# Kernel tuning notes

Hardware: AMD Instinct MI355X
Metric: run time of the kernel (lower is better)

## Reference

```python
import jax, jax.numpy as jnp
import numpy as np

D_MODEL = 1024
N_HEAD = 16
HEAD_DIM = D_MODEL // N_HEAD


def setup_inputs() -> dict:
    key = jax.random.key(0)
    k1, k2, k3 = jax.random.split(key, 3)
    B, T = 2, 2048
    x = jax.random.normal(k1, (B, T, D_MODEL), dtype=jnp.float32)
    # nn.MultiheadAttention packed in-projection: (3*D, D), xavier-like scale
    w_in = jax.random.normal(k2, (3 * D_MODEL, D_MODEL), dtype=jnp.float32) * (1.0 / np.sqrt(D_MODEL))
    b_in = jnp.zeros((3 * D_MODEL,), dtype=jnp.float32)
    w_out = jax.random.normal(k3, (D_MODEL, D_MODEL), dtype=jnp.float32) * (1.0 / np.sqrt(D_MODEL))
    b_out = jnp.zeros((D_MODEL,), dtype=jnp.float32)
    return {"x": x, "w_in": w_in, "b_in": b_in, "w_out": w_out, "b_out": b_out}


def reference(x, w_in, b_in, w_out, b_out):
    B, T, D = x.shape
    H, hd = N_HEAD, HEAD_DIM
    # packed QKV projection (torch Linear convention: y = x @ W.T + b)
    qkv = x @ w_in.T + b_in                      # [B, T, 3D]
    q, k, v = jnp.split(qkv, 3, axis=-1)
    # [B, H, T, hd]
    q = q.reshape(B, T, H, hd).transpose(0, 2, 1, 3)
    k = k.reshape(B, T, H, hd).transpose(0, 2, 1, 3)
    v = v.reshape(B, T, H, hd).transpose(0, 2, 1, 3)
    scale = 1.0 / np.sqrt(hd).astype(np.float32)
    scores = jnp.einsum("bhqd,bhkd->bhqk", q * scale, k)  # [B, H, T, T]
    causal = jnp.tril(jnp.ones((T, T), dtype=bool))
    scores = jnp.where(causal, scores, jnp.finfo(scores.dtype).min)
    attn = jax.nn.softmax(scores, axis=-1)
    ctx = jnp.einsum("bhqk,bhkd->bhqd", attn, v)           # [B, H, T, hd]
    ctx = ctx.transpose(0, 2, 1, 3).reshape(B, T, D)
    return ctx @ w_out.T + b_out
```

## Files before the change

kernel.cpp:

```cpp
#include <hip/hip_runtime.h>


#define T_SEQ 2048
#define D_MODEL 1024
#define NEG_BIG (-1.0e30f)
#define Q_SCALE 0.18033688f

typedef float f32x4 __attribute__((ext_vector_type(4)));
typedef short s16x8 __attribute__((ext_vector_type(8)));
typedef __bf16 bf16x8 __attribute__((ext_vector_type(8)));

__device__ __forceinline__ f32x4 mfma16(s16x8 a, s16x8 b, f32x4 c) {
    return __builtin_amdgcn_mfma_f32_16x16x32_bf16(
        __builtin_bit_cast(bf16x8, a), __builtin_bit_cast(bf16x8, b), c, 0, 0, 0);
}

__device__ __forceinline__ short f2bf(float f) {
    unsigned int u = __float_as_uint(f);
    u += 0x7fffu + ((u >> 16) & 1u);
    return (short)(u >> 16);
}
__device__ __forceinline__ float bf2f(short s) {
    return __uint_as_float(((unsigned int)(unsigned short)s) << 16);
}
__device__ __forceinline__ unsigned cvt_pk_bf16(float lo, float hi) {
    unsigned r;
    asm("v_cvt_pk_bf16_f32 %0, %1, %2" : "=v"(r) : "v"(lo), "v"(hi));
    return r;
}

__device__ __forceinline__ void async_lds16(const short* g, short* l) {
    __builtin_amdgcn_global_load_lds(
        (const __attribute__((address_space(1))) unsigned int*)g,
        (__attribute__((address_space(3))) unsigned int*)l, 16, 0, 0);
}

#define N_X   4194304
#define N_WI  3145728
#define N_BI  3072
#define N_WO  1048576
#define N_BO  1024
#define V_X   (N_X  / 4)
#define V_WI  (N_WI / 4)
#define V_BI  (N_BI / 4)
#define V_WO  (N_WO / 4)
#define V_BO  (N_BO / 4)
#define V_TOT (V_X + V_WI + V_BI + V_WO + V_BO)

__global__ __launch_bounds__(256) void canon_all_kernel(
    const float* __restrict__ x, const float* __restrict__ wi,
    const float* __restrict__ bi, const float* __restrict__ wo,
    const float* __restrict__ bo,
    short* __restrict__ xb, short* __restrict__ wib, short* __restrict__ bib,
    short* __restrict__ wob, short* __restrict__ bob)
{
    int i = blockIdx.x * 256 + threadIdx.x;
    if (i >= V_TOT) return;
    const float* src; short* dst; int off;
    if      (i < V_X)                    { src = x;  dst = xb;  off = i; }
    else if (i < V_X+V_WI)               { src = wi; dst = wib; off = i - V_X; }
    else if (i < V_X+V_WI+V_BI)          { src = bi; dst = bib; off = i - V_X - V_WI; }
    else if (i < V_X+V_WI+V_BI+V_WO)     { src = wo; dst = wob; off = i - V_X - V_WI - V_BI; }
    else                                 { src = bo; dst = bob; off = i - V_X - V_WI - V_BI - V_WO; }
    float4 v = ((const float4*)src)[off];
    short4 o = { f2bf(v.x), f2bf(v.y), f2bf(v.z), f2bf(v.w) };
    ((short4*)dst)[off] = o;
}

__global__ __launch_bounds__(512, 6) void gemm_qkv_kernel(
    const short* __restrict__ A, const short* __restrict__ B,
    const short* __restrict__ bias,
    short* __restrict__ qo, short* __restrict__ ko, short* __restrict__ vto)
{
    const int K = 1024;
    alignas(16) __shared__ short As[128][32];
    alignas(16) __shared__ short Bs[128][32];
    const int m0 = blockIdx.x * 128;
    const int n0 = blockIdx.y * 128;
    const int tid = threadIdx.x;
    const int lane = tid & 63;
    const int w = tid >> 6;
    const int wm = (w & 3) * 32;
    const int wn = (w >> 2) * 64;
    const int quad = lane >> 4, l16 = lane & 15;

    f32x4 acc[2][4];
    const f32x4 zero = {0.f, 0.f, 0.f, 0.f};
#pragma unroll
    for (int i = 0; i < 2; ++i)
#pragma unroll
        for (int j = 0; j < 4; ++j) acc[i][j] = zero;

    const int lrow = lane >> 2;
    const int lcol = (lane & 3) * 8;
    const short* gA = &A[(m0 + w*16 + lrow) * K + lcol];
    const short* gB = &B[(n0 + w*16 + lrow) * K + lcol];
    short* lA = &As[w*16][0];
    short* lB = &Bs[w*16][0];

    for (int k0 = 0; k0 < K; k0 += 32) {
        __syncthreads();
        async_lds16(gA + k0, lA);
        async_lds16(gB + k0, lB);
        __syncthreads();

        s16x8 af[2], bfr[4];
#pragma unroll
        for (int i = 0; i < 2; ++i) af[i]  = *(const s16x8*)&As[wm + i*16 + l16][quad*8];
#pragma unroll
        for (int j = 0; j < 4; ++j) bfr[j] = *(const s16x8*)&Bs[wn + j*16 + l16][quad*8];
#pragma unroll
        for (int i = 0; i < 2; ++i)
#pragma unroll
            for (int j = 0; j < 4; ++j)
                acc[i][j] = mfma16(af[i], bfr[j], acc[i][j]);
    }

#pragma unroll
    for (int j = 0; j < 4; ++j) {
        int n = n0 + wn + j*16 + l16;
        float bi = bf2f(bias[n]);
        int which = n >> 10;
        int h = (n >> 6) & 15, d = n & 63;
        if (which < 2) {
            short* dst = (which == 0) ? qo : ko;
            float scl = (which == 0) ? Q_SCALE : 1.0f;
#pragma unroll
            for (int i = 0; i < 2; ++i) {
#pragma unroll
                for (int r = 0; r < 4; ++r) {
                    int m = m0 + wm + i*16 + quad*4 + r;
                    int b = m >> 11, t = m & 2047;
                    float v = (acc[i][j][r] + bi) * scl;
                    dst[(((b*16 + h) * 2048) + t) * 64 + d] = f2bf(v);
                }
            }
        } else {
#pragma unroll
            for (int i = 0; i < 2; ++i) {
                int m = m0 + wm + i*16 + quad*4;
                int b = m >> 11, t0 = m & 2047;
                short4 o4 = { f2bf(acc[i][j][0] + bi), f2bf(acc[i][j][1] + bi),
                              f2bf(acc[i][j][2] + bi), f2bf(acc[i][j][3] + bi) };
                *(short4*)&vto[(((size_t)(b*16 + h) * 64) + d) * 2048 + t0] = o4;
            }
        }
    }
}

__global__ __launch_bounds__(512) void attn_kernel(
    const short* __restrict__ Q, const short* __restrict__ K,
    const short* __restrict__ Vt, short* __restrict__ ctx)
{
    alignas(16) __shared__ short Ks2[2][64][64];
    alignas(16) __shared__ short Vs2[2][64][64];
    alignas(16) __shared__ short Pl[8][16][72];

    const int bh = blockIdx.x;
    const int j  = blockIdx.y;
    const int tid = threadIdx.x;
    const int w = tid >> 6, lane = tid & 63;
    const int quad = lane >> 4, l16 = lane & 15;
    const int b = bh >> 4, h = bh & 15;

    const int isB = w >> 2;
    const int wq  = w & 3;
    const int qt  = isB ? (31 - j) : j;
    const int qbase  = qt * 64;
    const int qbaseA = j * 64;
    const int qbaseB = (31 - j) * 64;

    const short* Qb  = Q  + bh * T_SEQ * 64;
    const short* Kb  = K  + bh * T_SEQ * 64;
    const short* Vbt = Vt + (size_t)bh * 64 * T_SEQ;

    const int qg = qbase + wq*16 + l16;
    const short* qrow = Qb + qg * 64;
    const s16x8 qa0 = *(const s16x8*)(qrow + quad*8);
    const s16x8 qa1 = *(const s16x8*)(qrow + 32 + quad*8);

    const s16x8 ones = { (short)0x3F80, (short)0x3F80, (short)0x3F80, (short)0x3F80,
                         (short)0x3F80, (short)0x3F80, (short)0x3F80, (short)0x3F80 };

    const f32x4 zero = {0.f, 0.f, 0.f, 0.f};
    f32x4 o[4];
#pragma unroll
    for (int dt = 0; dt < 4; ++dt) o[dt] = zero;
    f32x4 ls = zero;

    const int srow   = w*8 + (lane >> 3);
    const int schunk = ((lane & 7) ^ (lane >> 3)) * 8;
    short* kdst0 = &Ks2[0][w*8][0];
    short* kdst1 = &Ks2[1][w*8][0];
    short* vdst0 = &Vs2[0][w*8][0];
    short* vdst1 = &Vs2[1][w*8][0];

    const int csw = (l16 & 7) * 8;

    async_lds16(&Kb[srow * 64 + schunk], kdst0);
    async_lds16(&Vbt[(size_t)srow * T_SEQ + schunk], vdst0);

    int cur = 0;
    for (int s0 = 0; s0 <= qbaseB; s0 += 64) {
        __syncthreads();

        if (s0 + 64 <= qbaseB) {
            async_lds16(&Kb[(s0 + 64 + srow) * 64 + schunk], cur ? kdst0 : kdst1);
            async_lds16(&Vbt[(size_t)srow * T_SEQ + s0 + 64 + schunk], cur ? vdst0 : vdst1);
        }

        const bool act = isB || (s0 <= qbaseA);
        if (act) {
#pragma unroll
            for (int sub = 0; sub < 4; ++sub) {
                s16x8 ka0 = *(const s16x8*)&Ks2[cur][sub*16 + l16][(quad*8) ^ csw];
                s16x8 ka1 = *(const s16x8*)&Ks2[cur][sub*16 + l16][(32 + quad*8) ^ csw];
                __builtin_amdgcn_s_setprio(1);
                f32x4 S = mfma16(ka1, qa1, mfma16(ka0, qa0, zero));
                __builtin_amdgcn_s_setprio(0);
                if (s0 == qbase) {
                    int sb = s0 + sub*16 + quad*4;
#pragma unroll
                    for (int r = 0; r < 4; ++r)
                        if (sb + r > qg) S[r] = NEG_BIG;
                }
                float p0 = exp2f(S[0]), p1 = exp2f(S[1]);
                float p2 = exp2f(S[2]), p3 = exp2f(S[3]);
                uint2 pk;
                pk.x = cvt_pk_bf16(p0, p1);
                pk.y = cvt_pk_bf16(p2, p3);
                *(uint2*)&Pl[w][l16][sub*16 + quad*4] = pk;
            }

            s16x8 pb0 = *(const s16x8*)&Pl[w][l16][quad*8];
            s16x8 pb1 = *(const s16x8*)&Pl[w][l16][32 + quad*8];
            __builtin_amdgcn_s_setprio(1);
            ls = mfma16(ones, pb1, mfma16(ones, pb0, ls));
#pragma unroll
            for (int dt = 0; dt < 4; ++dt) {
                s16x8 va0 = *(const s16x8*)&Vs2[cur][dt*16 + l16][(quad*8) ^ csw];
                s16x8 va1 = *(const s16x8*)&Vs2[cur][dt*16 + l16][(32 + quad*8) ^ csw];
                o[dt] = mfma16(va1, pb1, mfma16(va0, pb0, o[dt]));
            }
            __builtin_amdgcn_s_setprio(0);
        }
        cur ^= 1;
    }

    float inv = 1.0f / ls[0];
    int base = (b * T_SEQ + qg) * D_MODEL + h * 64;
#pragma unroll
    for (int dt = 0; dt < 4; ++dt) {
        uint2 pk;
        pk.x = cvt_pk_bf16(o[dt][0] * inv, o[dt][1] * inv);
        pk.y = cvt_pk_bf16(o[dt][2] * inv, o[dt][3] * inv);
        *(uint2*)&ctx[base + dt*16 + quad*4] = pk;
    }
}

__global__ __launch_bounds__(512, 4) void gemm_out_kernel(
    const short* __restrict__ A, const short* __restrict__ B,
    const short* __restrict__ bias, float* __restrict__ out)
{
    const int K = 1024;
    alignas(16) __shared__ short As[128][32];
    alignas(16) __shared__ short Bs[64][32];
    const int m0 = blockIdx.x * 128;
    const int n0 = blockIdx.y * 64;
    const int tid = threadIdx.x;
    const int lane = tid & 63;
    const int w = tid >> 6;
    const int wm = (w & 3) * 32;
    const int wn = (w >> 2) * 32;
    const int quad = lane >> 4, l16 = lane & 15;

    f32x4 acc[2][2];
    const f32x4 zero = {0.f, 0.f, 0.f, 0.f};
#pragma unroll
    for (int i = 0; i < 2; ++i)
#pragma unroll
        for (int j = 0; j < 2; ++j) acc[i][j] = zero;

    const int lrow = lane >> 2;
    const int lcol = (lane & 3) * 8;
    const short* gA = &A[(m0 + w*16 + lrow) * K + lcol];
    const short* gB = &B[(n0 + (w & 3)*16 + lrow) * K + lcol];
    short* lA = &As[w*16][0];
    short* lB = &Bs[(w & 3)*16][0];
    const bool stageB = (w < 4);

    for (int k0 = 0; k0 < K; k0 += 32) {
        __syncthreads();
        async_lds16(gA + k0, lA);
        if (stageB) async_lds16(gB + k0, lB);
        __syncthreads();

        s16x8 af[2], bfr[2];
#pragma unroll
        for (int i = 0; i < 2; ++i) af[i]  = *(const s16x8*)&As[wm + i*16 + l16][quad*8];
#pragma unroll
        for (int j = 0; j < 2; ++j) bfr[j] = *(const s16x8*)&Bs[wn + j*16 + l16][quad*8];
#pragma unroll
        for (int i = 0; i < 2; ++i)
#pragma unroll
            for (int j = 0; j < 2; ++j)
                acc[i][j] = mfma16(af[i], bfr[j], acc[i][j]);
    }

#pragma unroll
    for (int j = 0; j < 2; ++j) {
        int n = n0 + wn + j*16 + l16;
        float bi = bf2f(bias[n]);
#pragma unroll
        for (int i = 0; i < 2; ++i) {
#pragma unroll
            for (int r = 0; r < 4; ++r) {
                int m = m0 + wm + i*16 + quad*4 + r;
                out[m * 1024 + n] = acc[i][j][r] + bi;
            }
        }
    }
}

extern "C" void kernel_launch(void* const* d_in, const int* in_sizes, int n_in,
                              void* d_out, int out_size, void* d_ws, size_t ws_size,
                              hipStream_t stream) {
    float* out = (float*)d_out;
    char* ws = (char*)d_ws;

    const size_t MB = 1u << 20;
    short* xb     = (short*)(ws);
    short* w_inb  = (short*)(ws + 8*MB);
    short* b_inb  = (short*)(ws + 14*MB);
    short* w_outb = (short*)(ws + 15*MB);
    short* b_outb = (short*)(ws + 17*MB);
    short* qb     = (short*)(ws + 18*MB);
    short* kb     = (short*)(ws + 26*MB);
    short* vtb    = (short*)(ws + 34*MB);
    short* ctxb   = (short*)(ws + 42*MB);

    canon_all_kernel<<<(V_TOT + 255) / 256, 256, 0, stream>>>(
        (const float*)d_in[0], (const float*)d_in[1], (const float*)d_in[2],
        (const float*)d_in[3], (const float*)d_in[4],
        xb, w_inb, b_inb, w_outb, b_outb);

    gemm_qkv_kernel<<<dim3(32, 24), 512, 0, stream>>>(xb, w_inb, b_inb, qb, kb, vtb);
    attn_kernel<<<dim3(32, 16), 512, 0, stream>>>(qb, kb, vtb, ctxb);
    gemm_out_kernel<<<dim3(32, 16), 512, 0, stream>>>(ctxb, w_outb, b_outb, out);
}
```

Measured before the change: 172.0 us.

## Replace async double-buffered LDS loads with register-staged single buffer

Drops the async global-to-LDS double buffer with XOR swizzling in the attention kernel. K/V tiles are now prefetched into registers, written into a single padded LDS tile (row stride 72), and guarded by an extra barrier each iteration. This halves K/V shared memory and removes the swizzle arithmetic, but adds a second __syncthreads per tile and a register round-trip, which may reduce the overlap between loads and compute.

After: 174.2 us, median of 3. Within noise of the previous version (+1.3%).

```diff
diff --git a/kernel.cpp b/kernel.cpp
--- a/kernel.cpp
+++ b/kernel.cpp
@@ -152,8 +152,8 @@
     const short* __restrict__ Q, const short* __restrict__ K,
     const short* __restrict__ Vt, short* __restrict__ ctx)
 {
-    alignas(16) __shared__ short Ks2[2][64][64];
-    alignas(16) __shared__ short Vs2[2][64][64];
+    alignas(16) __shared__ short Ks[64][72];
+    alignas(16) __shared__ short Vs[64][72];
     alignas(16) __shared__ short Pl[8][16][72];
 
     const int bh = blockIdx.x;
@@ -188,33 +188,29 @@
     for (int dt = 0; dt < 4; ++dt) o[dt] = zero;
     f32x4 ls = zero;
 
-    const int srow   = w*8 + (lane >> 3);
-    const int schunk = ((lane & 7) ^ (lane >> 3)) * 8;
-    short* kdst0 = &Ks2[0][w*8][0];
-    short* kdst1 = &Ks2[1][w*8][0];
-    short* vdst0 = &Vs2[0][w*8][0];
-    short* vdst1 = &Vs2[1][w*8][0];
-
-    const int csw = (l16 & 7) * 8;
-
-    async_lds16(&Kb[srow * 64 + schunk], kdst0);
-    async_lds16(&Vbt[(size_t)srow * T_SEQ + schunk], vdst0);
-
-    int cur = 0;
+    const int sr  = tid >> 3;
+    const int scl = (tid & 7) * 8;
+
+    float4 kf = *(const float4*)&Kb[sr * 64 + scl];
+    float4 vf = *(const float4*)&Vbt[(size_t)sr * T_SEQ + scl];
+
     for (int s0 = 0; s0 <= qbaseB; s0 += 64) {
         __syncthreads();
+        *(float4*)&Ks[sr][scl] = kf;
+        *(float4*)&Vs[sr][scl] = vf;
+        __syncthreads();
 
         if (s0 + 64 <= qbaseB) {
-            async_lds16(&Kb[(s0 + 64 + srow) * 64 + schunk], cur ? kdst0 : kdst1);
-            async_lds16(&Vbt[(size_t)srow * T_SEQ + s0 + 64 + schunk], cur ? vdst0 : vdst1);
+            kf = *(const float4*)&Kb[(s0 + 64 + sr) * 64 + scl];
+            vf = *(const float4*)&Vbt[(size_t)sr * T_SEQ + s0 + 64 + scl];
         }
 
         const bool act = isB || (s0 <= qbaseA);
         if (act) {
 #pragma unroll
             for (int sub = 0; sub < 4; ++sub) {
-                s16x8 ka0 = *(const s16x8*)&Ks2[cur][sub*16 + l16][(quad*8) ^ csw];
-                s16x8 ka1 = *(const s16x8*)&Ks2[cur][sub*16 + l16][(32 + quad*8) ^ csw];
+                s16x8 ka0 = *(const s16x8*)&Ks[sub*16 + l16][quad*8];
+                s16x8 ka1 = *(const s16x8*)&Ks[sub*16 + l16][32 + quad*8];
                 __builtin_amdgcn_s_setprio(1);
                 f32x4 S = mfma16(ka1, qa1, mfma16(ka0, qa0, zero));
                 __builtin_amdgcn_s_setprio(0);
@@ -238,13 +234,12 @@
             ls = mfma16(ones, pb1, mfma16(ones, pb0, ls));
 #pragma unroll
             for (int dt = 0; dt < 4; ++dt) {
-                s16x8 va0 = *(const s16x8*)&Vs2[cur][dt*16 + l16][(quad*8) ^ csw];
-                s16x8 va1 = *(const s16x8*)&Vs2[cur][dt*16 + l16][(32 + quad*8) ^ csw];
+                s16x8 va0 = *(const s16x8*)&Vs[dt*16 + l16][quad*8];
+                s16x8 va1 = *(const s16x8*)&Vs[dt*16 + l16][32 + quad*8];
                 o[dt] = mfma16(va1, pb1, mfma16(va0, pb0, o[dt]));
             }
             __builtin_amdgcn_s_setprio(0);
         }
-        cur ^= 1;
     }
 
     float inv = 1.0f / ls[0];
```
